# Performance work log

Measured on AMD Instinct MI355X. Metric: run time of the kernel, lower is better.

## Reference

```python
import jax, jax.numpy as jnp
import numpy as np
from jax import lax

BETA = 0.9
THRESHOLD = 0.75
SLOPE = 25.0  # snntorch fast_sigmoid default slope
EPS = 1e-5

@jax.custom_vjp
def spike_fn(x):
    # Heaviside forward, fast-sigmoid surrogate backward
    return (x > 0).astype(x.dtype)

def _spike_fwd(x):
    return spike_fn(x), x

def _spike_bwd(x, g):
    return (g / (SLOPE * jnp.abs(x) + 1.0) ** 2,)

spike_fn.defvjp(_spike_fwd, _spike_bwd)

def lif_preprocess(spikes, W, b):
    """SpikeSequencePreprocessor: 1x1 conv mix + per-timestep Leaky LIF (subtract reset).
    spikes: [B, C, T] -> [B, C, T] binary spike trace."""
    mixed = jnp.einsum('oc,bct->tbo', W, spikes) + b[None, None, :]  # [T,B,C]
    zero = jnp.zeros_like(mixed[0])

    def step(carry, x_t):
        mem, spk = carry
        # snntorch Leaky subtract-reset: reset uses previous step's spike
        mem = BETA * mem + x_t - spk * THRESHOLD
        spk = spike_fn(mem - THRESHOLD)
        return (mem, spk), spk

    _, trace = lax.scan(step, (zero, zero), mixed)  # [T,B,C]
    return jnp.transpose(trace, (1, 2, 0))  # [B,C,T]

def layer_norm(x):
    mu = jnp.mean(x, axis=-1, keepdims=True)
    var = jnp.var(x, axis=-1, keepdims=True)
    return (x - mu) / jnp.sqrt(var + EPS)

def setup_inputs() -> dict:
    key = jax.random.key(0)
    ks = jax.random.split(key, 16)
    B, C, T, H = 64, 256, 1024, 512
    transmit = (jax.random.uniform(ks[0], (B, C, T)) < 0.2).astype(jnp.float32)
    receive = (jax.random.uniform(ks[1], (B, 2, C, T)) < 0.2).astype(jnp.float32)
    eye = jnp.eye(C, dtype=jnp.float32)
    return {
        'transmit_spikes': transmit,
        'receive_spikes': receive,
        'base_distance': jax.random.normal(ks[2], (B, H), jnp.float32),
        'base_azimuth': jax.random.normal(ks[3], (B, H), jnp.float32),
        'base_elevation': jax.random.normal(ks[4], (B, H), jnp.float32),
        'W_tx': eye + 0.01 * jax.random.normal(ks[5], (C, C), jnp.float32),
        'b_tx': jnp.zeros((C,), jnp.float32),
        'W_rx': eye + 0.01 * jax.random.normal(ks[6], (C, C), jnp.float32),
        'b_rx': jnp.zeros((C,), jnp.float32),
        'Wd': jax.random.normal(ks[7], (H, C), jnp.float32) / np.sqrt(C),
        'bd': jnp.zeros((H,), jnp.float32),
        'Wa': jax.random.normal(ks[8], (H, C), jnp.float32) / np.sqrt(C),
        'ba': jnp.zeros((H,), jnp.float32),
        'We': jax.random.normal(ks[9], (H, C), jnp.float32) / np.sqrt(C),
        'be': jnp.zeros((H,), jnp.float32),
        'gain_d': jnp.float32(-1.2),
        'gain_a': jnp.float32(-1.2),
        'gain_e': jnp.float32(-1.2),
    }

def reference(transmit_spikes, receive_spikes, base_distance, base_azimuth,
              base_elevation, W_tx, b_tx, W_rx, b_rx, Wd, bd, Wa, ba, We, be,
              gain_d, gain_a, gain_e):
    B, _, C, T = receive_spikes.shape
    tx = lif_preprocess(transmit_spikes, W_tx, b_tx)                 # [B,C,T]
    rx = lif_preprocess(receive_spikes.reshape(B * 2, C, T), W_rx, b_rx)
    rx = rx.reshape(B, 2, C, T)                                      # [B,2,C,T]
    left, right = rx[:, 0], rx[:, 1]

    # pathway features (stand-in for build_pathway_features): per-channel time reductions
    f_dist = jnp.mean(tx, axis=-1)            # [B,C]
    f_azi = jnp.mean(left - right, axis=-1)   # [B,C]
    f_ele = jnp.mean(left + right, axis=-1)   # [B,C]
    spike_proxy = jnp.sum(rx, axis=-1)        # [B,2,C]

    rd = layer_norm(f_dist) @ Wd.T + bd
    ra = layer_norm(f_azi) @ Wa.T + ba
    re = layer_norm(f_ele) @ We.T + be

    sd = 0.3 * jax.nn.sigmoid(gain_d)
    sa = 0.3 * jax.nn.sigmoid(gain_a)
    se = 0.3 * jax.nn.sigmoid(gain_e)

    distance_latent = jax.nn.relu(base_distance + sd * rd)
    azimuth_latent = jax.nn.relu(base_azimuth + sa * ra)
    elevation_latent = jax.nn.relu(base_elevation + se * re)
    return distance_latent, azimuth_latent, elevation_latent, rx, spike_proxy
```

## Files before the change

kernel.cpp:

```cpp
#include <hip/hip_runtime.h>

#define B_   64
#define C_   256
#define T_   1024
#define H_   512
#define G_   192

#define OUT_DIST 0
#define OUT_AZI  (64*512)
#define OUT_ELE  (2*64*512)
#define OUT_RX   (3*64*512)
#define OUT_SP   (3*64*512 + 64*2*256*1024)

typedef _Float16 half8  __attribute__((ext_vector_type(8)));
typedef float    floatx4 __attribute__((ext_vector_type(4)));

__global__ __launch_bounds__(256) void split_w(
    const float* __restrict__ Wtx, const float* __restrict__ Wrx,
    _Float16* __restrict__ w16)
{
    int e = blockIdx.x * 256 + threadIdx.x;
    int m = e >> 16;
    int i = e & 65535;
    float v = m ? Wrx[i] : Wtx[i];
    _Float16 hi = (_Float16)v;
    _Float16 lo = (_Float16)(v - (float)hi);
    w16[(size_t)m * 131072 + i] = hi;
    w16[(size_t)m * 131072 + 65536 + i] = lo;
}

#define STAGE_STORE(RS, BOFF)                                              \
    _Pragma("unroll")                                                      \
    for (int j = 0; j < 4; ++j) {                                          \
        int row = tq * 4 + j;                                              \
        half8 hv = { (_Float16)RS[0][j], (_Float16)RS[1][j],               \
                     (_Float16)RS[2][j], (_Float16)RS[3][j],               \
                     (_Float16)RS[4][j], (_Float16)RS[5][j],               \
                     (_Float16)RS[6][j], (_Float16)RS[7][j] };             \
        *(half8*)(sring + (BOFF) + (size_t)row * 72 + cq * 8) = hv;        \
    }

#define ISSUE_LOADS(RD, CBASE, TBASE) {                                    \
    const float* sb_ = Sg + (size_t)((CBASE) + cq * 8) * T_                \
                       + (TBASE) + tq * 4;                                 \
    _Pragma("unroll")                                                      \
    for (int i = 0; i < 8; ++i)                                            \
        RD[i] = *(const floatx4*)(sb_ + (size_t)i * T_); }

#define MFMA_QUARTER(QT, BOFF)                                             \
    _Pragma("unroll")                                                      \
    for (int ck2 = 0; ck2 < 2; ++ck2) {                                    \
        _Pragma("unroll")                                                  \
        for (int nt = 0; nt < 8; ++nt) {                                   \
            int row = nt * 16 + col;                                       \
            half8 bf = *(const half8*)(sring + (BOFF)                      \
                        + (size_t)row * 72 + ck2 * 32 + quad * 8);         \
            acc[nt] = __builtin_amdgcn_mfma_f32_16x16x32_f16(              \
                Ahi[(QT) * 2 + ck2], bf, acc[nt], 0, 0, 0);                \
            acc[nt] = __builtin_amdgcn_mfma_f32_16x16x32_f16(              \
                Alo[(QT) * 2 + ck2], bf, acc[nt], 0, 0, 0);                \
        }                                                                  \
    }

#define ROTATE_RING() { int bt_ = b0; b0 = b1; b1 = b2; b2 = bt_; }

__global__ __launch_bounds__(256, 2) void lif_mfma_v7(
    const float* __restrict__ transmit, const float* __restrict__ receive,
    const float* __restrict__ btx, const float* __restrict__ brx,
    const _Float16* __restrict__ w16, float* __restrict__ out,
    float* __restrict__ txCnt)
{
    __shared__ __align__(16) _Float16 sring[3 * 9216];

    const int tid = threadIdx.x;
    const int g   = blockIdx.x >> 2;
    const int ot  = blockIdx.x & 3;
    const int o0  = ot * 64;
    const bool isRx = (g >= 64);
    const int gr  = g - 64;

    const float* Sg = isRx ? (receive + (size_t)gr * C_ * T_)
                           : (transmit + (size_t)g * C_ * T_);
    const _Float16* whi = w16 + (isRx ? 131072 : 0);
    const _Float16* wlo = whi + 65536;
    const float* bp = isRx ? brx : btx;

    const int lane = tid & 63;
    const int wv   = tid >> 6;
    const int col  = lane & 15;
    const int quad = lane >> 4;

    const int oA = o0 + wv * 16 + col;
    half8 Ahi[8], Alo[8];
#pragma unroll
    for (int ck = 0; ck < 8; ++ck) {
        Ahi[ck] = *(const half8*)(whi + (size_t)oA * 256 + ck * 32 + quad * 8);
        Alo[ck] = *(const half8*)(wlo + (size_t)oA * 256 + ck * 32 + quad * 8);
    }
    floatx4 bias4 = *(const floatx4*)(bp + o0 + wv * 16 + quad * 4);

    const int tq = tid & 31;
    const int cq = tid >> 5;

    float mem = 0.f, spk = 0.f, cnt = 0.f;

    floatx4 rA[8], rB[8];
    floatx4 acc[8];

    ISSUE_LOADS(rA, 0, 0)
    ISSUE_LOADS(rB, 64, 0)
    STAGE_STORE(rA, 0)
    __syncthreads();

    int b0 = 0, b1 = 9216, b2 = 18432;

    for (int tt = 0; tt < 8; ++tt) {
#pragma unroll
        for (int nt = 0; nt < 8; ++nt) acc[nt] = bias4;

        STAGE_STORE(rB, b1)
        __syncthreads();
        ISSUE_LOADS(rA, 2 * 64, tt * 128)
        MFMA_QUARTER(0, b0)
        __syncthreads();
        ROTATE_RING()

        STAGE_STORE(rA, b1)
        __syncthreads();
        ISSUE_LOADS(rB, 3 * 64, tt * 128)
        MFMA_QUARTER(1, b0)
        __syncthreads();
        ROTATE_RING()

        STAGE_STORE(rB, b1)
        __syncthreads();
        if (tt < 7) ISSUE_LOADS(rA, 0, (tt + 1) * 128)
        MFMA_QUARTER(2, b0)
        __syncthreads();
        ROTATE_RING()

        if (tt < 7) { STAGE_STORE(rA, b1) }
        __syncthreads();
        if (tt < 7) ISSUE_LOADS(rB, 64, (tt + 1) * 128)
        MFMA_QUARTER(3, b0)
        __syncthreads();

        {
            float* E = (float*)(sring + b0);
#pragma unroll
            for (int h = 0; h < 2; ++h) {
#pragma unroll
                for (int ntl = 0; ntl < 4; ++ntl) {
                    int tl = ntl * 16 + col;
                    *(floatx4*)(E + (size_t)tl * 72 + wv * 16 + quad * 4) =
                        acc[h * 4 + ntl];
                }
                __syncthreads();

                if ((tid & 63) < 16) {
                    const int oloc = wv * 16 + (tid & 15);
                    if (isRx) {
#pragma unroll 8
                        for (int t = 0; t < 64; ++t) {
                            float x = E[t * 72 + oloc];
                            mem = 0.9f * mem + x - spk * 0.75f;
                            spk = (mem > 0.75f) ? 1.0f : 0.0f;
                            cnt += spk;
                            E[t * 72 + oloc] = spk;
                        }
                    } else {
#pragma unroll 8
                        for (int t = 0; t < 64; ++t) {
                            float x = E[t * 72 + oloc];
                            mem = 0.9f * mem + x - spk * 0.75f;
                            spk = (mem > 0.75f) ? 1.0f : 0.0f;
                            cnt += spk;
                        }
                    }
                }
                __syncthreads();

                if (isRx) {
                    const int olane = tid >> 2;
                    const int tl4   = (tid & 3) * 4;
                    float* drow = out + (size_t)OUT_RX + (size_t)gr * C_ * T_
                                  + (size_t)(o0 + olane) * T_
                                  + tt * 128 + h * 64;
#pragma unroll
                    for (int q = 0; q < 4; ++q) {
                        int t = tl4 + q * 16;
                        float4 v = make_float4(E[(t + 0) * 72 + olane],
                                               E[(t + 1) * 72 + olane],
                                               E[(t + 2) * 72 + olane],
                                               E[(t + 3) * 72 + olane]);
                        *(float4*)(drow + t) = v;
                    }
                }
                __syncthreads();
            }
        }
        ROTATE_RING()
    }

    if ((tid & 63) < 16) {
        const int og = o0 + wv * 16 + (tid & 15);
        if (isRx) out[(size_t)OUT_SP + (size_t)gr * 256 + og] = cnt;
        else      txCnt[(size_t)g * 256 + og] = cnt;
    }
}

__global__ __launch_bounds__(128) void lif_gemm_scan(
    const float* __restrict__ transmit, const float* __restrict__ receive,
    const float* __restrict__ Wtx, const float* __restrict__ btx,
    const float* __restrict__ Wrx, const float* __restrict__ brx,
    float* __restrict__ out, float* __restrict__ wsF)
{
    __shared__ float lds[128 * 68];
    float* Slds = lds;
    float* Wlds = lds + 4096;
    float* Mlds = lds;

    const int tid = threadIdx.x;
    const int bx  = blockIdx.x;
    const int ot  = bx / G_;
    const int g   = bx % G_;
    const int o0  = ot * 64;
    const bool isRx = (g >= 64);

    const float* Sg = isRx ? (receive + (size_t)(g - 64) * C_ * T_)
                           : (transmit + (size_t)g * C_ * T_);
    const float* Wp = isRx ? Wrx : Wtx;
    const float* bp = isRx ? brx : btx;

    const int ti = tid & 15;
    const int oi = tid >> 4;
    const int tb = ti * 4;
    const int ob = oi * 4;

    float bias[2][4];
#pragma unroll
    for (int os = 0; os < 2; ++os)
#pragma unroll
        for (int j = 0; j < 4; ++j)
            bias[os][j] = bp[o0 + os * 32 + ob + j];

    float mem = 0.f, spk = 0.f, cnt = 0.f;

    for (int tt = 0; tt < 8; ++tt) {
        const int t0 = tt * 128;
        float acc[8][8];
#pragma unroll
        for (int ii = 0; ii < 8; ++ii)
#pragma unroll
            for (int jj = 0; jj < 8; ++jj)
                acc[ii][jj] = bias[jj >> 2][jj & 3];

        for (int kk = 0; kk < 8; ++kk) {
            const int c0 = kk * 32;
#pragma unroll
            for (int p = 0; p < 8; ++p) {
                int idx = tid + p * 128;
                int c = idx >> 5, t4 = idx & 31;
                *(float4*)(Slds + c * 128 + t4 * 4) =
                    *(const float4*)(Sg + (size_t)(c0 + c) * T_ + t0 + t4 * 4);
            }
#pragma unroll
            for (int p = 0; p < 4; ++p) {
                int idx = tid + p * 128;
                int o = idx >> 3, c4 = idx & 7;
                float4 w = *(const float4*)(Wp + (size_t)(o0 + o) * C_ + c0 + c4 * 4);
                Wlds[(c4 * 4 + 0) * 64 + o] = w.x;
                Wlds[(c4 * 4 + 1) * 64 + o] = w.y;
                Wlds[(c4 * 4 + 2) * 64 + o] = w.z;
                Wlds[(c4 * 4 + 3) * 64 + o] = w.w;
            }
            __syncthreads();
#pragma unroll 8
            for (int k = 0; k < 32; ++k) {
                float4 a0 = *(const float4*)(Slds + k * 128 + tb);
                float4 a1 = *(const float4*)(Slds + k * 128 + 64 + tb);
                float4 b0 = *(const float4*)(Wlds + k * 64 + ob);
                float4 b1 = *(const float4*)(Wlds + k * 64 + 32 + ob);
                float a[8]  = {a0.x, a0.y, a0.z, a0.w, a1.x, a1.y, a1.z, a1.w};
                float bv[8] = {b0.x, b0.y, b0.z, b0.w, b1.x, b1.y, b1.z, b1.w};
#pragma unroll
                for (int ii = 0; ii < 8; ++ii)
#pragma unroll
                    for (int jj = 0; jj < 8; ++jj)
                        acc[ii][jj] += a[ii] * bv[jj];
            }
            __syncthreads();
        }

#pragma unroll
        for (int ii = 0; ii < 8; ++ii) {
            int t = (ii >> 2) * 64 + tb + (ii & 3);
#pragma unroll
            for (int os = 0; os < 2; ++os) {
                float4 v = make_float4(acc[ii][os * 4 + 0], acc[ii][os * 4 + 1],
                                       acc[ii][os * 4 + 2], acc[ii][os * 4 + 3]);
                *(float4*)(Mlds + t * 68 + os * 32 + ob) = v;
            }
        }
        __syncthreads();

        if (tid < 64) {
#pragma unroll 4
            for (int t = 0; t < 128; ++t) {
                float x = Mlds[t * 68 + tid];
                mem = 0.9f * mem + x - spk * 0.75f;
                spk = (mem > 0.75f) ? 1.0f : 0.0f;
                cnt += spk;
                Mlds[t * 68 + tid] = spk;
            }
        }
        __syncthreads();

        if (isRx) {
            float* dst = out + (size_t)OUT_RX + (size_t)(g - 64) * C_ * T_
                         + (size_t)o0 * T_ + t0;
            int m = tid & 7;
            int orow0 = tid >> 3;
#pragma unroll
            for (int p = 0; p < 4; ++p) {
                int orow = orow0 + p * 16;
#pragma unroll
                for (int q = 0; q < 4; ++q) {
                    int tq = m * 4 + q * 32;
                    float4 v = make_float4(Mlds[(tq + 0) * 68 + orow],
                                           Mlds[(tq + 1) * 68 + orow],
                                           Mlds[(tq + 2) * 68 + orow],
                                           Mlds[(tq + 3) * 68 + orow]);
                    *(float4*)(dst + (size_t)orow * T_ + tq) = v;
                }
            }
        }
        __syncthreads();
    }

    if (tid < 64) {
        if (isRx) out[(size_t)OUT_SP + (size_t)(g - 64) * C_ + o0 + tid] = cnt;
        else      wsF[(size_t)g * C_ + o0 + tid] = cnt;
    }
}

__global__ __launch_bounds__(256) void heads_kernel(
    const float* __restrict__ wsF, const float* __restrict__ sp,
    const float* __restrict__ Wd, const float* __restrict__ bd,
    const float* __restrict__ Wa, const float* __restrict__ ba,
    const float* __restrict__ We, const float* __restrict__ be,
    const float* __restrict__ gd, const float* __restrict__ ga, const float* __restrict__ ge,
    const float* __restrict__ based, const float* __restrict__ basea, const float* __restrict__ basee,
    float* __restrict__ out)
{
    __shared__ float fv[256];
    __shared__ float red[8];
    const int tid = threadIdx.x;
    const int hd  = blockIdx.x >> 6;
    const int b   = blockIdx.x & 63;

    float f;
    if (hd == 0) {
        f = wsF[b * 256 + tid] * (1.f / 1024.f);
    } else {
        float l = sp[(2 * b) * 256 + tid];
        float r = sp[(2 * b + 1) * 256 + tid];
        f = ((hd == 1) ? (l - r) : (l + r)) * (1.f / 1024.f);
    }

    float v = f;
#pragma unroll
    for (int off = 32; off > 0; off >>= 1) v += __shfl_down(v, off, 64);
    if ((tid & 63) == 0) red[tid >> 6] = v;
    __syncthreads();
    float mu = (red[0] + red[1] + red[2] + red[3]) * (1.f / 256.f);

    float d = f - mu;
    v = d * d;
#pragma unroll
    for (int off = 32; off > 0; off >>= 1) v += __shfl_down(v, off, 64);
    if ((tid & 63) == 0) red[4 + (tid >> 6)] = v;
    __syncthreads();
    float var  = (red[4] + red[5] + red[6] + red[7]) * (1.f / 256.f);
    float rstd = rsqrtf(var + 1e-5f);
    fv[tid] = d * rstd;
    __syncthreads();

    const float* W    = (hd == 0) ? Wd : (hd == 1) ? Wa : We;
    const float* bb   = (hd == 0) ? bd : (hd == 1) ? ba : be;
    const float* base = (hd == 0) ? based : (hd == 1) ? basea : basee;
    float gain = (hd == 0) ? gd[0] : (hd == 1) ? ga[0] : ge[0];
    float s = 0.3f / (1.f + expf(-gain));

    const float4* fv4 = (const float4*)fv;
#pragma unroll
    for (int hh = 0; hh < 2; ++hh) {
        int h = tid + hh * 256;
        const float4* W4 = (const float4*)(W + (size_t)h * 256);
        float acc = 0.f;
#pragma unroll 8
        for (int c = 0; c < 64; ++c) {
            float4 w = W4[c];
            float4 x = fv4[c];
            acc += w.x * x.x + w.y * x.y + w.z * x.z + w.w * x.w;
        }
        float r = acc + bb[h];
        float o = base[b * 512 + h] + s * r;
        out[(size_t)hd * (64 * 512) + b * 512 + h] = fmaxf(o, 0.f);
    }
}

extern "C" void kernel_launch(void* const* d_in, const int* in_sizes, int n_in,
                              void* d_out, int out_size, void* d_ws, size_t ws_size,
                              hipStream_t stream)
{
    const float* transmit = (const float*)d_in[0];
    const float* receive  = (const float*)d_in[1];
    const float* based    = (const float*)d_in[2];
    const float* basea    = (const float*)d_in[3];
    const float* basee    = (const float*)d_in[4];
    const float* Wtx      = (const float*)d_in[5];
    const float* btx      = (const float*)d_in[6];
    const float* Wrx      = (const float*)d_in[7];
    const float* brx      = (const float*)d_in[8];
    const float* Wd       = (const float*)d_in[9];
    const float* bd       = (const float*)d_in[10];
    const float* Wa       = (const float*)d_in[11];
    const float* ba       = (const float*)d_in[12];
    const float* We       = (const float*)d_in[13];
    const float* be       = (const float*)d_in[14];
    const float* gd       = (const float*)d_in[15];
    const float* ga       = (const float*)d_in[16];
    const float* ge       = (const float*)d_in[17];
    float* out = (float*)d_out;
    float* spOut = out + (size_t)OUT_SP;

    const size_t need = 512 * 1024 + 64 * 1024;

    if (ws_size >= need) {
        _Float16* w16   = (_Float16*)d_ws;
        float*    txCnt = (float*)d_ws + 131072;

        hipLaunchKernelGGL(split_w, dim3(512), dim3(256), 0, stream,
                           Wtx, Wrx, w16);
        hipLaunchKernelGGL(lif_mfma_v7, dim3(768), dim3(256), 0, stream,
                           transmit, receive, btx, brx, w16, out, txCnt);
        hipLaunchKernelGGL(heads_kernel, dim3(192), dim3(256), 0, stream,
                           txCnt, spOut, Wd, bd, Wa, ba, We, be,
                           gd, ga, ge, based, basea, basee, out);
    } else {
        float* wsF = (float*)d_ws;
        hipLaunchKernelGGL(lif_gemm_scan, dim3(768), dim3(128), 0, stream,
                           transmit, receive, Wtx, btx, Wrx, brx, out, wsF);
        hipLaunchKernelGGL(heads_kernel, dim3(192), dim3(256), 0, stream,
                           wsF, spOut, Wd, bd, Wa, ba, We, be,
                           gd, ga, ge, based, basea, basee, out);
    }
}
```

Before: 439.0 us.

## Replace padded LDS rows with XOR swizzle, raise occupancy, reorder block mapping

Drops the 72-element padded LDS row stride and uses a dense 64-element stride with an XOR swizzle on 16-byte chunks, applied consistently to the staging stores, the MFMA B-operand reads, the epilogue accumulator writes, the scan and the rx writeback. This shrinks the LDS ring, and launch bounds are raised to 3 blocks per CU to allow higher occupancy. The block index mapping now places the 64-channel output tile in the slow index, so consecutive blocks handle different batch groups while sharing the same weight slice. Risks are extra index arithmetic in the serial scan loop and register pressure from the 3-block bound, which could cause spills.

```diff
diff --git a/kernel.cpp b/kernel.cpp
--- a/kernel.cpp
+++ b/kernel.cpp
@@ -33,11 +33,12 @@
     _Pragma("unroll")                                                      \
     for (int j = 0; j < 4; ++j) {                                          \
         int row = tq * 4 + j;                                              \
+        int phys = cq ^ ((row >> 1) & 7);                                  \
         half8 hv = { (_Float16)RS[0][j], (_Float16)RS[1][j],               \
                      (_Float16)RS[2][j], (_Float16)RS[3][j],               \
                      (_Float16)RS[4][j], (_Float16)RS[5][j],               \
                      (_Float16)RS[6][j], (_Float16)RS[7][j] };             \
-        *(half8*)(sring + (BOFF) + (size_t)row * 72 + cq * 8) = hv;        \
+        *(half8*)(sring + (BOFF) + (size_t)row * 64 + 8 * phys) = hv;      \
     }
 
 #define ISSUE_LOADS(RD, CBASE, TBASE) {                                    \
@@ -53,8 +54,9 @@
         _Pragma("unroll")                                                  \
         for (int nt = 0; nt < 8; ++nt) {                                   \
             int row = nt * 16 + col;                                       \
+            int phys = (ck2 * 4 + quad) ^ ((row >> 1) & 7);                \
             half8 bf = *(const half8*)(sring + (BOFF)                      \
-                        + (size_t)row * 72 + ck2 * 32 + quad * 8);         \
+                        + (size_t)row * 64 + 8 * phys);                    \
             acc[nt] = __builtin_amdgcn_mfma_f32_16x16x32_f16(              \
                 Ahi[(QT) * 2 + ck2], bf, acc[nt], 0, 0, 0);                \
             acc[nt] = __builtin_amdgcn_mfma_f32_16x16x32_f16(              \
@@ -64,17 +66,17 @@
 
 #define ROTATE_RING() { int bt_ = b0; b0 = b1; b1 = b2; b2 = bt_; }
 
-__global__ __launch_bounds__(256, 2) void lif_mfma_v7(
+__global__ __launch_bounds__(256, 3) void lif_mfma_v8(
     const float* __restrict__ transmit, const float* __restrict__ receive,
     const float* __restrict__ btx, const float* __restrict__ brx,
     const _Float16* __restrict__ w16, float* __restrict__ out,
     float* __restrict__ txCnt)
 {
-    __shared__ __align__(16) _Float16 sring[3 * 9216];
+    __shared__ __align__(16) _Float16 sring[3 * 8192];
 
     const int tid = threadIdx.x;
-    const int g   = blockIdx.x >> 2;
-    const int ot  = blockIdx.x & 3;
+    const int ot  = blockIdx.x / G_;
+    const int g   = blockIdx.x % G_;
     const int o0  = ot * 64;
     const bool isRx = (g >= 64);
     const int gr  = g - 64;
@@ -112,7 +114,7 @@
     STAGE_STORE(rA, 0)
     __syncthreads();
 
-    int b0 = 0, b1 = 9216, b2 = 18432;
+    int b0 = 0, b1 = 8192, b2 = 16384;
 
     for (int tt = 0; tt < 8; ++tt) {
 #pragma unroll
@@ -152,26 +154,29 @@
 #pragma unroll
                 for (int ntl = 0; ntl < 4; ++ntl) {
                     int tl = ntl * 16 + col;
-                    *(floatx4*)(E + (size_t)tl * 72 + wv * 16 + quad * 4) =
-                        acc[h * 4 + ntl];
+                    int ph = (wv * 4 + quad) ^ ((tl >> 1) & 7);
+                    *(floatx4*)(E + (size_t)tl * 64 + 4 * ph) = acc[h * 4 + ntl];
                 }
                 __syncthreads();
 
                 if ((tid & 63) < 16) {
                     const int oloc = wv * 16 + (tid & 15);
+                    const int oq = oloc >> 2, ol = oloc & 3;
                     if (isRx) {
 #pragma unroll 8
                         for (int t = 0; t < 64; ++t) {
-                            float x = E[t * 72 + oloc];
+                            int idx = t * 64 + 4 * (oq ^ ((t >> 1) & 7)) + ol;
+                            float x = E[idx];
                             mem = 0.9f * mem + x - spk * 0.75f;
                             spk = (mem > 0.75f) ? 1.0f : 0.0f;
                             cnt += spk;
-                            E[t * 72 + oloc] = spk;
+                            E[idx] = spk;
                         }
                     } else {
 #pragma unroll 8
                         for (int t = 0; t < 64; ++t) {
-                            float x = E[t * 72 + oloc];
+                            int idx = t * 64 + 4 * (oq ^ ((t >> 1) & 7)) + ol;
+                            float x = E[idx];
                             mem = 0.9f * mem + x - spk * 0.75f;
                             spk = (mem > 0.75f) ? 1.0f : 0.0f;
                             cnt += spk;
@@ -183,16 +188,18 @@
                 if (isRx) {
                     const int olane = tid >> 2;
                     const int tl4   = (tid & 3) * 4;
+                    const int oq = olane >> 2, ol = olane & 3;
                     float* drow = out + (size_t)OUT_RX + (size_t)gr * C_ * T_
                                   + (size_t)(o0 + olane) * T_
                                   + tt * 128 + h * 64;
 #pragma unroll
                     for (int q = 0; q < 4; ++q) {
                         int t = tl4 + q * 16;
-                        float4 v = make_float4(E[(t + 0) * 72 + olane],
-                                               E[(t + 1) * 72 + olane],
-                                               E[(t + 2) * 72 + olane],
-                                               E[(t + 3) * 72 + olane]);
+                        float4 v = make_float4(
+                            E[(t + 0) * 64 + 4 * (oq ^ (((t + 0) >> 1) & 7)) + ol],
+                            E[(t + 1) * 64 + 4 * (oq ^ (((t + 1) >> 1) & 7)) + ol],
+                            E[(t + 2) * 64 + 4 * (oq ^ (((t + 2) >> 1) & 7)) + ol],
+                            E[(t + 3) * 64 + 4 * (oq ^ (((t + 3) >> 1) & 7)) + ol]);
                         *(float4*)(drow + t) = v;
                     }
                 }
@@ -443,7 +450,7 @@
 
         hipLaunchKernelGGL(split_w, dim3(512), dim3(256), 0, stream,
                            Wtx, Wrx, w16);
-        hipLaunchKernelGGL(lif_mfma_v7, dim3(768), dim3(256), 0, stream,
+        hipLaunchKernelGGL(lif_mfma_v8, dim3(768), dim3(256), 0, stream,
                            transmit, receive, btx, brx, w16, out, txCnt);
         hipLaunchKernelGGL(heads_kernel, dim3(192), dim3(256), 0, stream,
                            txCnt, spOut, Wd, bd, Wa, ba, We, be,
```

New measurement: 455.0 us. +3.6%, slower.
